# Kernel tuning notes

Hardware: AMD Instinct MI355X
Metric: run time of the kernel (lower is better)

The kernel has to match this reference:

```python
import jax, jax.numpy as jnp
import numpy as np

NUM_INPUTS = 4096
K = 64
BATCH = 16384


def setup_inputs() -> dict:
    key = jax.random.key(0)
    X = jax.random.normal(key, (BATCH, NUM_INPUTS), dtype=jnp.float32)
    return {"X": X}


def reference(X):
    # Per-row (1 - k/n) quantile of |X| (linear interpolation, matching
    # torch.quantile default), then soft-threshold preserving sign.
    q = 1.0 - K / NUM_INPUTS
    X_abs = jnp.abs(X)
    Q = jnp.quantile(X_abs, q, axis=1, method="linear")  # [batch]
    X_trunc = jnp.maximum(X_abs - Q[:, None], 0.0)
    return jnp.sign(X) * X_trunc
```

## Files before the change

### kernel.cpp

```cpp
#include <hip/hip_runtime.h>
#include <cstdint>

constexpr int NCOLS   = 4096;
constexpr int THREADS = 256;
constexpr int EPT     = NCOLS / THREADS;
constexpr int KSEL    = 65;

__device__ __forceinline__ float soft(float x, float Q) {
    float r = fmaxf(fabsf(x) - Q, 0.0f);
    return copysignf(r, x);
}

__global__ __launch_bounds__(THREADS) void topk_sparsify(
    const float* __restrict__ X, float* __restrict__ out, int rows)
{
    const int row = blockIdx.x;
    if (row >= rows) return;
    const int t = threadIdx.x;

    const float4* __restrict__ x4 = reinterpret_cast<const float4*>(X + (size_t)row * NCOLS);
    float4* __restrict__       o4 = reinterpret_cast<float4*>(out + (size_t)row * NCOLS);

    float4 d[4];
#pragma unroll
    for (int i = 0; i < 4; ++i) d[i] = x4[t + THREADS * i];

    uint32_t a[EPT];
#pragma unroll
    for (int i = 0; i < 4; ++i) {
        a[4*i+0] = __float_as_uint(d[i].x) & 0x7FFFFFFFu;
        a[4*i+1] = __float_as_uint(d[i].y) & 0x7FFFFFFFu;
        a[4*i+2] = __float_as_uint(d[i].z) & 0x7FFFFFFFu;
        a[4*i+3] = __float_as_uint(d[i].w) & 0x7FFFFFFFu;
    }

    __shared__ uint32_t hist[2048];
    __shared__ uint32_t scan[THREADS];
    __shared__ uint32_t sel_digit_s;
    __shared__ uint32_t sel_k_s;
    __shared__ uint32_t wcnt[4], wmn[4];
    __shared__ float    q_sh;

    uint32_t known = 0;
    uint32_t k     = KSEL;

    const int      shifts[3] = {20, 10, 0};
    const uint32_t dmask [3] = {0x7FFu, 0x3FFu, 0x3FFu};
    const int      nbins [3] = {2048, 1024, 1024};
    const uint32_t pmask [3] = {0u, 0xFFF00000u, 0xFFFFFC00u};

#pragma unroll
    for (int p = 0; p < 3; ++p) {
        const int      sh = shifts[p];
        const uint32_t dm = dmask[p];
        const int      nb = nbins[p];
        const uint32_t pm = pmask[p];

        for (int b = t; b < nb; b += THREADS) hist[b] = 0u;
        __syncthreads();

#pragma unroll
        for (int i = 0; i < EPT; ++i) {
            if ((a[i] & pm) == known) {
                atomicAdd(&hist[(a[i] >> sh) & dm], 1u);
            }
        }
        __syncthreads();

        const int gpb  = nb / THREADS;
        const int base = t * gpb;
        uint32_t gsum = 0;
        for (int j = 0; j < gpb; ++j) gsum += hist[base + j];
        scan[t] = gsum;
        __syncthreads();

        for (int off = 1; off < THREADS; off <<= 1) {
            uint32_t val = scan[t];
            if (t + off < THREADS) val += scan[t + off];
            __syncthreads();
            scan[t] = val;
            __syncthreads();
        }
        const uint32_t above = (t + 1 < THREADS) ? scan[t + 1] : 0u;

        uint32_t G = above;
        for (int j = gpb - 1; j >= 0; --j) {
            const uint32_t c = hist[base + j];
            if (G < k && k <= G + c) {
                sel_digit_s = (uint32_t)(base + j);
                sel_k_s     = k - G;
            }
            G += c;
        }
        __syncthreads();
        known |= sel_digit_s << sh;
        k = sel_k_s;
        __syncthreads();
    }

    const uint32_t b65 = known;
    const float    v65 = __uint_as_float(b65);

    uint32_t cnt = 0, mn = 0xFFFFFFFFu;
#pragma unroll
    for (int i = 0; i < EPT; ++i) {
        if (a[i] > b65) { cnt++; mn = min(mn, a[i]); }
    }
#pragma unroll
    for (int off = 32; off >= 1; off >>= 1) {
        cnt += __shfl_down(cnt, off, 64);
        uint32_t m2 = __shfl_down(mn, off, 64);
        mn = min(mn, m2);
    }
    const int wave = t >> 6, lane = t & 63;
    if (lane == 0) { wcnt[wave] = cnt; wmn[wave] = mn; }
    __syncthreads();
    if (t == 0) {
        uint32_t C = wcnt[0] + wcnt[1] + wcnt[2] + wcnt[3];
        uint32_t M = min(min(wmn[0], wmn[1]), min(wmn[2], wmn[3]));
        float v64 = (C == 64u) ? __uint_as_float(M) : v65;
        q_sh = fmaf(0.015625f, v64 - v65, v65);
    }
    __syncthreads();
    const float Q = q_sh;

#pragma unroll
    for (int i = 0; i < 4; ++i) {
        float4 f = d[i];
        f.x = soft(f.x, Q);
        f.y = soft(f.y, Q);
        f.z = soft(f.z, Q);
        f.w = soft(f.w, Q);
        o4[t + THREADS * i] = f;
    }
}

extern "C" void kernel_launch(void* const* d_in, const int* in_sizes, int n_in,
                              void* d_out, int out_size, void* d_ws, size_t ws_size,
                              hipStream_t stream) {
    const float* X  = (const float*)d_in[0];
    float*       out = (float*)d_out;
    const int rows = in_sizes[0] / NCOLS;
    topk_sparsify<<<rows, THREADS, 0, stream>>>(X, out, rows);
}
```

Before: 440.5 us.

## Replace radix-select histogram with sigma-guided threshold and candidate binary search

Drops the three-pass LDS histogram radix select. An initial threshold is estimated from the row RMS and adjusted until between 65 and 256 elements exceed it. Those candidates are compacted into shared memory and a single wave binary-searches the 65th largest value. A full binary search over the float bit range is the fallback. Sign bits are packed so the float4 registers need not stay live, which cuts atomics, syncs and register pressure. The heuristic's convergence depends on the input distribution, and the fallback path is slower.

New measurement: 447.1 us. About the same (+1.5%).

```diff
diff --git a/kernel.cpp b/kernel.cpp
--- a/kernel.cpp
+++ b/kernel.cpp
@@ -3,143 +3,168 @@
 
 constexpr int NCOLS   = 4096;
 constexpr int THREADS = 256;
-constexpr int EPT     = NCOLS / THREADS;
-constexpr int KSEL    = 65;
-
-__device__ __forceinline__ float soft(float x, float Q) {
-    float r = fmaxf(fabsf(x) - Q, 0.0f);
-    return copysignf(r, x);
-}
+constexpr int EPT     = 16;
+constexpr int CAP     = 256;
 
 __global__ __launch_bounds__(THREADS) void topk_sparsify(
-    const float* __restrict__ X, float* __restrict__ out, int rows)
+    const float* __restrict__ X, float* __restrict__ out)
 {
-    const int row = blockIdx.x;
-    if (row >= rows) return;
-    const int t = threadIdx.x;
+    const int row  = blockIdx.x;
+    const int t    = threadIdx.x;
+    const int wave = t >> 6;
+    const int lane = t & 63;
 
-    const float4* __restrict__ x4 = reinterpret_cast<const float4*>(X + (size_t)row * NCOLS);
-    float4* __restrict__       o4 = reinterpret_cast<float4*>(out + (size_t)row * NCOLS);
+    __shared__ uint32_t wsum[4];
+    __shared__ float    fsum[4];
+    __shared__ uint32_t cand[CAP];
 
-    float4 d[4];
-#pragma unroll
-    for (int i = 0; i < 4; ++i) d[i] = x4[t + THREADS * i];
+    const float4* __restrict__ x4 =
+        reinterpret_cast<const float4*>(X + (size_t)row * NCOLS);
+    float4* __restrict__ o4 = reinterpret_cast<float4*>(out + (size_t)row * NCOLS);
 
     uint32_t a[EPT];
+    uint32_t sbits = 0;
+    float ss = 0.0f;
 #pragma unroll
     for (int i = 0; i < 4; ++i) {
-        a[4*i+0] = __float_as_uint(d[i].x) & 0x7FFFFFFFu;
-        a[4*i+1] = __float_as_uint(d[i].y) & 0x7FFFFFFFu;
-        a[4*i+2] = __float_as_uint(d[i].z) & 0x7FFFFFFFu;
-        a[4*i+3] = __float_as_uint(d[i].w) & 0x7FFFFFFFu;
+        float4 v = x4[t + THREADS * i];
+        uint32_t u0 = __float_as_uint(v.x), u1 = __float_as_uint(v.y);
+        uint32_t u2 = __float_as_uint(v.z), u3 = __float_as_uint(v.w);
+        a[4*i+0] = u0 & 0x7FFFFFFFu;  a[4*i+1] = u1 & 0x7FFFFFFFu;
+        a[4*i+2] = u2 & 0x7FFFFFFFu;  a[4*i+3] = u3 & 0x7FFFFFFFu;
+        sbits |= (u0 >> 31) << (4*i+0);
+        sbits |= (u1 >> 31) << (4*i+1);
+        sbits |= (u2 >> 31) << (4*i+2);
+        sbits |= (u3 >> 31) << (4*i+3);
+        ss = fmaf(v.x, v.x, ss); ss = fmaf(v.y, v.y, ss);
+        ss = fmaf(v.z, v.z, ss); ss = fmaf(v.w, v.w, ss);
     }
 
-    __shared__ uint32_t hist[2048];
-    __shared__ uint32_t scan[THREADS];
-    __shared__ uint32_t sel_digit_s;
-    __shared__ uint32_t sel_k_s;
-    __shared__ uint32_t wcnt[4], wmn[4];
-    __shared__ float    q_sh;
+#pragma unroll
+    for (int off = 32; off >= 1; off >>= 1) ss += __shfl_xor(ss, off, 64);
+    if (lane == 0) fsum[wave] = ss;
+    __syncthreads();
+    const float sigma = sqrtf(fsum[0] + fsum[1] + fsum[2] + fsum[3]) * (1.0f / 64.0f);
 
-    uint32_t known = 0;
-    uint32_t k     = KSEL;
+    float T = 2.1f * sigma;
+    uint32_t tb = 0, C = 0, myc = 0;
+    bool ok = false;
+    for (int it = 0; it < 16; ++it) {
+        tb  = __float_as_uint(T);
+        myc = 0;
+#pragma unroll
+        for (int i = 0; i < EPT; ++i) myc += (a[i] > tb) ? 1u : 0u;
+        uint32_t c = myc;
+#pragma unroll
+        for (int off = 32; off >= 1; off >>= 1) c += __shfl_xor(c, off, 64);
+        __syncthreads();
+        if (lane == 0) wsum[wave] = c;
+        __syncthreads();
+        C = wsum[0] + wsum[1] + wsum[2] + wsum[3];
+        if (C >= 65u && C <= (uint32_t)CAP) { ok = true; break; }
+        T = (C < 65u) ? T * 0.70f : T * 1.35f;
+    }
 
-    const int      shifts[3] = {20, 10, 0};
-    const uint32_t dmask [3] = {0x7FFu, 0x3FFu, 0x3FFu};
-    const int      nbins [3] = {2048, 1024, 1024};
-    const uint32_t pmask [3] = {0u, 0xFFF00000u, 0xFFFFFC00u};
-
+    uint32_t b65;
+    if (ok) {
+        uint32_t pre = myc;
 #pragma unroll
-    for (int p = 0; p < 3; ++p) {
-        const int      sh = shifts[p];
-        const uint32_t dm = dmask[p];
-        const int      nb = nbins[p];
-        const uint32_t pm = pmask[p];
-
-        for (int b = t; b < nb; b += THREADS) hist[b] = 0u;
+        for (int off = 1; off < 64; off <<= 1) {
+            uint32_t v = __shfl_up(pre, off, 64);
+            if (lane >= off) pre += v;
+        }
+        uint32_t wtot = __shfl(pre, 63, 64);
+        __syncthreads();
+        if (lane == 0) wsum[wave] = wtot;
+        __syncthreads();
+        uint32_t base = 0;
+#pragma unroll
+        for (int w = 0; w < 4; ++w) base += (w < wave) ? wsum[w] : 0u;
+        uint32_t o = base + pre - myc;
+#pragma unroll
+        for (int i = 0; i < EPT; ++i)
+            if (a[i] > tb) cand[o++] = a[i];
         __syncthreads();
 
+        uint32_t r0 = (lane        < (int)C) ? cand[lane      ] : 0u;
+        uint32_t r1 = (lane + 64   < (int)C) ? cand[lane +  64] : 0u;
+        uint32_t r2 = (lane + 128  < (int)C) ? cand[lane + 128] : 0u;
+        uint32_t r3 = (lane + 192  < (int)C) ? cand[lane + 192] : 0u;
+
+        uint32_t mx = max(max(r0, r1), max(r2, r3));
 #pragma unroll
-        for (int i = 0; i < EPT; ++i) {
-            if ((a[i] & pm) == known) {
-                atomicAdd(&hist[(a[i] >> sh) & dm], 1u);
-            }
+        for (int off = 32; off >= 1; off >>= 1)
+            mx = max(mx, (uint32_t)__shfl_xor(mx, off, 64));
+
+        uint32_t lo = tb + 1u, hi = mx;
+        while (lo < hi) {
+            uint32_t mid = lo + ((hi - lo) >> 1);
+            uint32_t c = ((r0 > mid) ? 1u : 0u) + ((r1 > mid) ? 1u : 0u) +
+                         ((r2 > mid) ? 1u : 0u) + ((r3 > mid) ? 1u : 0u);
+#pragma unroll
+            for (int off = 32; off >= 1; off >>= 1) c += __shfl_xor(c, off, 64);
+            if (c < 65u) hi = mid; else lo = mid + 1u;
         }
-        __syncthreads();
-
-        const int gpb  = nb / THREADS;
-        const int base = t * gpb;
-        uint32_t gsum = 0;
-        for (int j = 0; j < gpb; ++j) gsum += hist[base + j];
-        scan[t] = gsum;
-        __syncthreads();
-
-        for (int off = 1; off < THREADS; off <<= 1) {
-            uint32_t val = scan[t];
-            if (t + off < THREADS) val += scan[t + off];
+        b65 = lo;
+    } else {
+        uint32_t lo = 0u, hi = 0x7F800000u;
+        while (lo < hi) {
+            uint32_t mid = lo + ((hi - lo) >> 1);
+            uint32_t c = 0;
+#pragma unroll
+            for (int i = 0; i < EPT; ++i) c += (a[i] > mid) ? 1u : 0u;
+#pragma unroll
+            for (int off = 32; off >= 1; off >>= 1) c += __shfl_xor(c, off, 64);
             __syncthreads();
-            scan[t] = val;
+            if (lane == 0) wsum[wave] = c;
             __syncthreads();
+            uint32_t tot = wsum[0] + wsum[1] + wsum[2] + wsum[3];
+            if (tot < 65u) hi = mid; else lo = mid + 1u;
         }
-        const uint32_t above = (t + 1 < THREADS) ? scan[t + 1] : 0u;
-
-        uint32_t G = above;
-        for (int j = gpb - 1; j >= 0; --j) {
-            const uint32_t c = hist[base + j];
-            if (G < k && k <= G + c) {
-                sel_digit_s = (uint32_t)(base + j);
-                sel_k_s     = k - G;
-            }
-            G += c;
-        }
-        __syncthreads();
-        known |= sel_digit_s << sh;
-        k = sel_k_s;
-        __syncthreads();
+        b65 = lo;
     }
-
-    const uint32_t b65 = known;
-    const float    v65 = __uint_as_float(b65);
 
     uint32_t cnt = 0, mn = 0xFFFFFFFFu;
 #pragma unroll
     for (int i = 0; i < EPT; ++i) {
-        if (a[i] > b65) { cnt++; mn = min(mn, a[i]); }
+        bool g = a[i] > b65;
+        cnt += g ? 1u : 0u;
+        mn = min(mn, g ? a[i] : 0xFFFFFFFFu);
     }
 #pragma unroll
     for (int off = 32; off >= 1; off >>= 1) {
-        cnt += __shfl_down(cnt, off, 64);
-        uint32_t m2 = __shfl_down(mn, off, 64);
-        mn = min(mn, m2);
-    }
-    const int wave = t >> 6, lane = t & 63;
-    if (lane == 0) { wcnt[wave] = cnt; wmn[wave] = mn; }
-    __syncthreads();
-    if (t == 0) {
-        uint32_t C = wcnt[0] + wcnt[1] + wcnt[2] + wcnt[3];
-        uint32_t M = min(min(wmn[0], wmn[1]), min(wmn[2], wmn[3]));
-        float v64 = (C == 64u) ? __uint_as_float(M) : v65;
-        q_sh = fmaf(0.015625f, v64 - v65, v65);
+        cnt += __shfl_xor(cnt, off, 64);
+        mn = min(mn, (uint32_t)__shfl_xor(mn, off, 64));
     }
     __syncthreads();
-    const float Q = q_sh;
+    if (lane == 0) { wsum[wave] = cnt; fsum[wave] = __uint_as_float(mn); }
+    __syncthreads();
+    const uint32_t Ct = wsum[0] + wsum[1] + wsum[2] + wsum[3];
+    const uint32_t M  = min(min(__float_as_uint(fsum[0]), __float_as_uint(fsum[1])),
+                            min(__float_as_uint(fsum[2]), __float_as_uint(fsum[3])));
+    const float v65 = __uint_as_float(b65);
+    const float v64 = (Ct == 64u) ? __uint_as_float(M) : v65;
+    const float Q = fmaf(0.015625f, v64 - v65, v65);
 
 #pragma unroll
     for (int i = 0; i < 4; ++i) {
-        float4 f = d[i];
-        f.x = soft(f.x, Q);
-        f.y = soft(f.y, Q);
-        f.z = soft(f.z, Q);
-        f.w = soft(f.w, Q);
-        o4[t + THREADS * i] = f;
+        float r[4];
+#pragma unroll
+        for (int j = 0; j < 4; ++j) {
+            const int idx = 4*i + j;
+            float mag = fmaxf(__uint_as_float(a[idx]) - Q, 0.0f);
+            uint32_t bits = __float_as_uint(mag) | (((sbits >> idx) & 1u) << 31);
+            r[j] = __uint_as_float(bits);
+        }
+        o4[t + THREADS * i] = make_float4(r[0], r[1], r[2], r[3]);
     }
 }
 
 extern "C" void kernel_launch(void* const* d_in, const int* in_sizes, int n_in,
                               void* d_out, int out_size, void* d_ws, size_t ws_size,
                               hipStream_t stream) {
-    const float* X  = (const float*)d_in[0];
+    const float* X   = (const float*)d_in[0];
     float*       out = (float*)d_out;
     const int rows = in_sizes[0] / NCOLS;
-    topk_sparsify<<<rows, THREADS, 0, stream>>>(X, out, rows);
+    topk_sparsify<<<rows, THREADS, 0, stream>>>(X, out);
 }
```
